# Kernel tuning notes

Measured on AMD Instinct MI355X. Metric: run time of the kernel, lower is better.

## Reference

```python
import jax, jax.numpy as jnp
import numpy as np

EPS = 1e-12
N_POS, N_NEG, N_NEUT, N_ASSAS = 9, 8, 7, 1
VOCAB_K = 512  # vocab_size: number of search results
NEUT_W, NEG_W, ASSAS_W = 1.0, 0.0, -10.0


def _normalize(x):
    # F.normalize(p=2, dim=-1)
    return x / jnp.maximum(jnp.linalg.norm(x, axis=-1, keepdims=True), EPS)


def _pool(embs):
    # mean over dim 1, then L2-normalize
    return _normalize(jnp.mean(embs, axis=1))


def setup_inputs() -> dict:
    key = jax.random.key(0)
    ks = jax.random.split(key, 10)
    B = 64
    inp = {
        "pos_embs": jax.random.normal(ks[0], (B, N_POS, 768), jnp.float32),
        "neg_embs": jax.random.normal(ks[1], (B, N_NEG, 768), jnp.float32),
        "neut_embs": jax.random.normal(ks[2], (B, N_NEUT, 768), jnp.float32),
        "assas_emb": jax.random.normal(ks[3], (B, 768), jnp.float32),
        "vocab_table": jax.random.normal(ks[4], (100000, 768), jnp.float32),
        "W1": jax.random.normal(ks[5], (3072, 2304), jnp.float32) * 0.02,
        "b1": jnp.zeros((2304,), jnp.float32),
        "W2": jax.random.normal(ks[6], (2304, 1700), jnp.float32) * 0.02,
        "b2": jnp.zeros((1700,), jnp.float32),
        "W3": jax.random.normal(ks[7], (1700, 1000), jnp.float32) * 0.02,
        "b3": jnp.zeros((1000,), jnp.float32),
        "W4": jax.random.normal(ks[8], (1000, 768), jnp.float32) * 0.02,
        "b4": jnp.zeros((768,), jnp.float32),
    }
    return inp


def _forward(pos_embs, neg_embs, neut_embs, assas_emb, vocab_table,
             W1, b1, W2, b2, W3, b3, W4, b4):
    # --- combined input: cat(neg_pool, assas, neut_pool, pos_pool) -> [B, 3072]
    concatenated = jnp.concatenate(
        [_pool(neg_embs), assas_emb, _pool(neut_embs), _pool(pos_embs)], axis=1)

    # --- fc MLP with tanh activations (none after last layer)
    h = jnp.tanh(concatenated @ W1 + b1)
    h = jnp.tanh(h @ W2 + b2)
    h = jnp.tanh(h @ W3 + b3)
    model_out = _normalize(h @ W4 + b4)  # [B, 768]

    # --- vocab.search: top-VOCAB_K cosine similarity against vocab table
    vocab_norm = _normalize(vocab_table)            # [N, 768]
    sims = model_out @ vocab_norm.T                  # [B, N]
    _, top_idx = jax.lax.top_k(sims, VOCAB_K)        # [B, V]
    word_embeddings = vocab_table[top_idx]           # [B, V, 768]

    # --- cosine scores against each board group (normalize then dot)
    wn = _normalize(word_embeddings)                 # [B, V, 768]
    pos_s = jnp.einsum('bvd,bpd->bvp', wn, _normalize(pos_embs))    # [B,V,9]
    neg_s = jnp.einsum('bvd,bpd->bvp', wn, _normalize(neg_embs))    # [B,V,8]
    neut_s = jnp.einsum('bvd,bpd->bvp', wn, _normalize(neut_embs))  # [B,V,7]
    assas_s = jnp.einsum('bvd,bd->bv', wn, _normalize(assas_emb))[..., None]  # [B,V,1]

    # --- primary reward: # of positive words ranked before first non-positive
    combined = jnp.concatenate([pos_s, neg_s, neut_s, assas_s], axis=2)  # [B,V,25]
    order = jnp.argsort(-combined, axis=2)           # descending sort indices
    reward_vec = jnp.concatenate(
        [jnp.zeros((N_POS,), jnp.float32),
         jnp.ones((N_NEG + N_NEUT + N_ASSAS,), jnp.float32)])
    rewards = reward_vec[order]                      # [B,V,25]
    primary = jnp.argmax(rewards, axis=2).astype(jnp.float32)  # [B,V]

    # --- secondary reward: weight of the highest-scoring non-positive word
    combined2 = combined[:, :, N_POS:]               # [B,V,16]
    reward_vec2 = jnp.concatenate(
        [jnp.full((N_NEG,), NEG_W, jnp.float32),
         jnp.full((N_NEUT,), NEUT_W, jnp.float32),
         jnp.full((N_ASSAS,), ASSAS_W, jnp.float32)])
    secondary = reward_vec2[jnp.argmax(combined2, axis=2)]      # [B,V]

    tot_reward = primary + secondary                 # [B,V]

    # --- topk(V//2) max / min selection, gather, mean-pool, normalize
    k = VOCAB_K // 2
    _, idx_max = jax.lax.top_k(tot_reward, k)
    _, idx_min = jax.lax.top_k(-tot_reward, k)
    emb_max = jnp.take_along_axis(word_embeddings, idx_max[:, :, None], axis=1)
    emb_min = jnp.take_along_axis(word_embeddings, idx_min[:, :, None], axis=1)
    max_pooled = _pool(emb_max)
    min_pooled = _pool(emb_min)
    search_embedding = emb_max[:, 0]                 # highest-scoring embedding

    return model_out, search_embedding, max_pooled, min_pooled


def reference(pos_embs, neg_embs, neut_embs, assas_emb, vocab_table,
              W1, b1, W2, b2, W3, b3, W4, b4):
    return _forward(pos_embs, neg_embs, neut_embs, assas_emb, vocab_table,
                    W1, b1, W2, b2, W3, b3, W4, b4)
```

## Files before the change

kernel.cpp:

```cpp
#include <hip/hip_runtime.h>
#include <hip/hip_bf16.h>
#include <stdint.h>

#define B_    64
#define D_    768
#define NVOC  100000
#define VK    512
#define KH    256

__device__ __forceinline__ float b2f_raw(unsigned short u) {
    return __uint_as_float(((unsigned int)u) << 16);
}
__device__ __forceinline__ float ldin(const void* p, size_t i, int isbf) {
    return isbf ? b2f_raw(((const unsigned short*)p)[i]) : ((const float*)p)[i];
}
__device__ __forceinline__ float4 ldin4(const void* p, size_t i, int isbf) {
    if (isbf) {
        ushort4 r = *(const ushort4*)((const unsigned short*)p + i);
        return make_float4(b2f_raw(r.x), b2f_raw(r.y), b2f_raw(r.z), b2f_raw(r.w));
    }
    return *(const float4*)((const float*)p + i);
}
__device__ __forceinline__ uint32_t fmono(float x) {
    uint32_t u = __float_as_uint(x);
    return u ^ (uint32_t)((((int32_t)u) >> 31) | 0x80000000u);
}

__device__ __forceinline__ float block_reduce_sum_256(float v, float* red) {
    int tid = threadIdx.x;
    red[tid] = v; __syncthreads();
    #pragma unroll
    for (int s = 128; s > 0; s >>= 1) {
        if (tid < s) red[tid] += red[tid + s];
        __syncthreads();
    }
    float r = red[0]; __syncthreads();
    return r;
}

__global__ void detect_kernel(const void* vocab, int* flag) {
    if (threadIdx.x == 0 && blockIdx.x == 0) {
        const float* vf = (const float*)vocab;
        int sane = 0;
        for (int i = 0; i < 256; i++) {
            float a = fabsf(vf[i]);
            if (a > 1e-4f && a < 64.0f) sane++;
        }
        *flag = (sane >= 200) ? 0 : 1;
    }
}

__global__ __launch_bounds__(256) void prep_kernel(
    const void* __restrict__ pos, const void* __restrict__ neg,
    const void* __restrict__ neut, const void* __restrict__ assas,
    float* __restrict__ concat, float* __restrict__ invemb,
    const int* __restrict__ dflag) {
    __shared__ float red[256];
    int isbf = *dflag;
    int b = blockIdx.x, tid = threadIdx.x;
    int d = tid * 3;
    const void* srcs[3] = {pos, neg, neut};
    const int cnts[3]  = {9, 8, 7};
    const int ieoff[3] = {0, 9, 17};
    const int coff[3]  = {2304, 0, 1536};
    for (int g = 0; g < 3; g++) {
        float m0 = 0.f, m1 = 0.f, m2 = 0.f;
        int cnt = cnts[g];
        for (int m = 0; m < cnt; m++) {
            size_t base = ((size_t)b * cnt + m) * D_ + d;
            float x0 = ldin(srcs[g], base + 0, isbf);
            float x1 = ldin(srcs[g], base + 1, isbf);
            float x2 = ldin(srcs[g], base + 2, isbf);
            float S = block_reduce_sum_256(x0 * x0 + x1 * x1 + x2 * x2, red);
            if (tid == 0)
                invemb[b * 25 + ieoff[g] + m] = 1.0f / fmaxf(sqrtf(S), 1e-12f);
            m0 += x0; m1 += x1; m2 += x2;
        }
        float invc = 1.0f / (float)cnt;
        m0 *= invc; m1 *= invc; m2 *= invc;
        float S = block_reduce_sum_256(m0 * m0 + m1 * m1 + m2 * m2, red);
        float inv = 1.0f / fmaxf(sqrtf(S), 1e-12f);
        float* o = concat + (size_t)b * 3072 + coff[g] + d;
        o[0] = m0 * inv; o[1] = m1 * inv; o[2] = m2 * inv;
    }
    size_t abase = (size_t)b * D_ + d;
    float x0 = ldin(assas, abase + 0, isbf);
    float x1 = ldin(assas, abase + 1, isbf);
    float x2 = ldin(assas, abase + 2, isbf);
    float* oc = concat + (size_t)b * 3072 + 768 + d;
    oc[0] = x0; oc[1] = x1; oc[2] = x2;
    float S = block_reduce_sum_256(x0 * x0 + x1 * x1 + x2 * x2, red);
    if (tid == 0) invemb[b * 25 + 24] = 1.0f / fmaxf(sqrtf(S), 1e-12f);
}

__global__ __launch_bounds__(256) void gemm_partial_kernel(
    const float* __restrict__ X, const void* __restrict__ W,
    float* __restrict__ P, int K, int N, int CH, const int* __restrict__ dflag) {
    __shared__ float xs[64][68];
    __shared__ float wt[64][68];
    int isbf = *dflag;
    int tid = threadIdx.x;
    int n0 = blockIdx.x * 64;
    int kstart = blockIdx.y * CH;
    int kend = min(K, kstart + CH);
    int tx = tid & 15, ty = tid >> 4;
    float acc[4][4] = {{0.f}};
    for (int k0 = kstart; k0 < kend; k0 += 64) {
        #pragma unroll
        for (int q = 0; q < 4; q++) {
            int e4 = tid + q * 256;
            int m = e4 >> 4, kk = (e4 & 15) * 4;
            float4 v = make_float4(0.f, 0.f, 0.f, 0.f);
            if (k0 + kk < kend) v = *(const float4*)(X + (size_t)m * K + k0 + kk);
            xs[kk + 0][m] = v.x; xs[kk + 1][m] = v.y;
            xs[kk + 2][m] = v.z; xs[kk + 3][m] = v.w;
        }
        #pragma unroll
        for (int q = 0; q < 4; q++) {
            int e4 = tid + q * 256;
            int kk = e4 >> 4, c = (e4 & 15) * 4;
            float4 v = make_float4(0.f, 0.f, 0.f, 0.f);
            if (k0 + kk < kend && n0 + c < N)
                v = ldin4(W, (size_t)(k0 + kk) * N + n0 + c, isbf);
            wt[kk][c + 0] = v.x; wt[kk][c + 1] = v.y;
            wt[kk][c + 2] = v.z; wt[kk][c + 3] = v.w;
        }
        __syncthreads();
        #pragma unroll 16
        for (int kk = 0; kk < 64; kk++) {
            float4 a = *(const float4*)&xs[kk][ty * 4];
            float4 w = *(const float4*)&wt[kk][tx * 4];
            acc[0][0] += a.x * w.x; acc[0][1] += a.x * w.y; acc[0][2] += a.x * w.z; acc[0][3] += a.x * w.w;
            acc[1][0] += a.y * w.x; acc[1][1] += a.y * w.y; acc[1][2] += a.y * w.z; acc[1][3] += a.y * w.w;
            acc[2][0] += a.z * w.x; acc[2][1] += a.z * w.y; acc[2][2] += a.z * w.z; acc[2][3] += a.z * w.w;
            acc[3][0] += a.w * w.x; acc[3][1] += a.w * w.y; acc[3][2] += a.w * w.z; acc[3][3] += a.w * w.w;
        }
        __syncthreads();
    }
    size_t base = (size_t)blockIdx.y * 64 * N;
    int n = n0 + tx * 4;
    if (n < N) {
        #pragma unroll
        for (int i = 0; i < 4; i++) {
            float4 o = make_float4(acc[i][0], acc[i][1], acc[i][2], acc[i][3]);
            *(float4*)(P + base + (size_t)(ty * 4 + i) * N + n) = o;
        }
    }
}

__global__ __launch_bounds__(256) void reduce_act_kernel(
    const float* __restrict__ P, const void* __restrict__ bias,
    float* __restrict__ Y, int N, int KS, int act, const int* __restrict__ dflag) {
    int isbf = *dflag;
    int idx = blockIdx.x * 256 + threadIdx.x;
    if (idx >= 64 * N) return;
    int n = idx % N;
    float s = 0.f;
    for (int ks = 0; ks < KS; ks++) s += P[(size_t)ks * 64 * N + idx];
    s += ldin(bias, n, isbf);
    if (act) s = tanhf(s);
    Y[idx] = s;
}

__global__ __launch_bounds__(256) void norm_mo_kernel(
    float* __restrict__ mo, float* __restrict__ out, float* __restrict__ moTp) {
    __shared__ float red[256];
    int b = blockIdx.x, tid = threadIdx.x, d = tid * 3;
    float* r_ = mo + (size_t)b * D_ + d;
    float x0 = r_[0], x1 = r_[1], x2 = r_[2];
    float S = block_reduce_sum_256(x0 * x0 + x1 * x1 + x2 * x2, red);
    float inv = 1.0f / fmaxf(sqrtf(S), 1e-12f);
    x0 *= inv; x1 *= inv; x2 *= inv;
    r_[0] = x0; r_[1] = x1; r_[2] = x2;
    float* o = out + (size_t)b * D_ + d;
    o[0] = x0; o[1] = x1; o[2] = x2;
    if (moTp) {
        moTp[(size_t)(d + 0) * 64 + b] = x0;
        moTp[(size_t)(d + 1) * 64 + b] = x1;
        moTp[(size_t)(d + 2) * 64 + b] = x2;
    }
}

__global__ __launch_bounds__(256) void sims64_kernel(
    const float* __restrict__ moT, const void* __restrict__ vocab,
    float* __restrict__ sims, float* __restrict__ invn,
    const int* __restrict__ dflag) {
    __shared__ float xs[64 * 64];
    __shared__ float wt[64 * 64];
    int isbf = *dflag;
    int tid = threadIdx.x;
    int v0 = blockIdx.x * 64;
    int tx = tid & 15, ty = tid >> 4;
    float acc[4][4] = {{0.f}};
    float ssq[4] = {0.f, 0.f, 0.f, 0.f};
    for (int k0 = 0; k0 < 768; k0 += 64) {
        #pragma unroll
        for (int q = 0; q < 4; q++) {
            int e4 = tid + q * 256;
            int kr = e4 >> 4, m4 = (e4 & 15) * 4;
            float4 v = *(const float4*)(moT + (size_t)(k0 + kr) * 64 + m4);
            *(float4*)&xs[kr * 64 + m4] = v;
        }
        #pragma unroll
        for (int q = 0; q < 4; q++) {
            int e4 = tid + q * 256;
            int r = e4 >> 4, kq = e4 & 15, c = kq * 4;
            float4 v = make_float4(0.f, 0.f, 0.f, 0.f);
            if (v0 + r < NVOC)
                v = ldin4(vocab, (size_t)(v0 + r) * 768 + k0 + c, isbf);
            int colp = r ^ ((kq & 7) << 2);
            wt[(c + 0) * 64 + colp] = v.x;
            wt[(c + 1) * 64 + colp] = v.y;
            wt[(c + 2) * 64 + colp] = v.z;
            wt[(c + 3) * 64 + colp] = v.w;
        }
        __syncthreads();
        #pragma unroll 16
        for (int kk = 0; kk < 64; kk++) {
            float4 a = *(const float4*)&xs[kk * 64 + ty * 4];
            float4 w = *(const float4*)&wt[kk * 64 + ((tx * 4) ^ (((kk >> 2) & 7) << 2))];
            ssq[0] += w.x * w.x; ssq[1] += w.y * w.y; ssq[2] += w.z * w.z; ssq[3] += w.w * w.w;
            acc[0][0] += a.x * w.x; acc[0][1] += a.x * w.y; acc[0][2] += a.x * w.z; acc[0][3] += a.x * w.w;
            acc[1][0] += a.y * w.x; acc[1][1] += a.y * w.y; acc[1][2] += a.y * w.z; acc[1][3] += a.y * w.w;
            acc[2][0] += a.z * w.x; acc[2][1] += a.z * w.y; acc[2][2] += a.z * w.z; acc[2][3] += a.z * w.w;
            acc[3][0] += a.w * w.x; acc[3][1] += a.w * w.y; acc[3][2] += a.w * w.z; acc[3][3] += a.w * w.w;
        }
        __syncthreads();
    }
    int v = v0 + tx * 4;
    if (v < NVOC) {
        float inv[4];
        #pragma unroll
        for (int j = 0; j < 4; j++) inv[j] = 1.0f / fmaxf(sqrtf(ssq[j]), 1e-12f);
        #pragma unroll
        for (int i = 0; i < 4; i++) {
            float4 o = make_float4(acc[i][0] * inv[0], acc[i][1] * inv[1],
                                   acc[i][2] * inv[2], acc[i][3] * inv[3]);
            *(float4*)(sims + (size_t)(ty * 4 + i) * NVOC + v) = o;
        }
        if (ty == 0) *(float4*)(invn + v) = make_float4(inv[0], inv[1], inv[2], inv[3]);
    }
}

__global__ __launch_bounds__(256) void sims_kernel(
    const float* __restrict__ mo32, const void* __restrict__ vocab,
    float* __restrict__ sims, float* __restrict__ invn, int winv,
    const int* __restrict__ dflag) {
    __shared__ float xs[64][36];
    __shared__ float wt[64][68];
    int isbf = *dflag;
    int tid = threadIdx.x;
    int v0 = blockIdx.x * 64;
    int tx = tid & 15, ty = tid >> 4;
    float acc[2][4] = {{0.f}};
    float ssq[4] = {0.f, 0.f, 0.f, 0.f};
    for (int k0 = 0; k0 < 768; k0 += 64) {
        #pragma unroll
        for (int q = 0; q < 2; q++) {
            int e4 = tid + q * 256;
            int m = e4 >> 4, kk = (e4 & 15) * 4;
            float4 v = *(const float4*)(mo32 + (size_t)m * 768 + k0 + kk);
            xs[kk + 0][m] = v.x; xs[kk + 1][m] = v.y;
            xs[kk + 2][m] = v.z; xs[kk + 3][m] = v.w;
        }
        #pragma unroll
        for (int q = 0; q < 4; q++) {
            int e4 = tid + q * 256;
            int r = e4 >> 4, c = (e4 & 15) * 4;
            float4 v = make_float4(0.f, 0.f, 0.f, 0.f);
            if (v0 + r < NVOC)
                v = ldin4(vocab, (size_t)(v0 + r) * 768 + k0 + c, isbf);
            wt[c + 0][r] = v.x; wt[c + 1][r] = v.y;
            wt[c + 2][r] = v.z; wt[c + 3][r] = v.w;
        }
        __syncthreads();
        #pragma unroll 16
        for (int kk = 0; kk < 64; kk++) {
            float2 a = *(const float2*)&xs[kk][ty * 2];
            float4 w = *(const float4*)&wt[kk][tx * 4];
            ssq[0] += w.x * w.x; ssq[1] += w.y * w.y; ssq[2] += w.z * w.z; ssq[3] += w.w * w.w;
            acc[0][0] += a.x * w.x; acc[0][1] += a.x * w.y; acc[0][2] += a.x * w.z; acc[0][3] += a.x * w.w;
            acc[1][0] += a.y * w.x; acc[1][1] += a.y * w.y; acc[1][2] += a.y * w.z; acc[1][3] += a.y * w.w;
        }
        __syncthreads();
    }
    int v = v0 + tx * 4;
    if (v < NVOC) {
        float inv[4];
        #pragma unroll
        for (int j = 0; j < 4; j++) inv[j] = 1.0f / fmaxf(sqrtf(ssq[j]), 1e-12f);
        #pragma unroll
        for (int i = 0; i < 2; i++) {
            float4 o = make_float4(acc[i][0] * inv[0], acc[i][1] * inv[1],
                                   acc[i][2] * inv[2], acc[i][3] * inv[3]);
            *(float4*)(sims + (size_t)(ty * 2 + i) * NVOC + v) = o;
        }
        if (ty == 0 && winv) *(float4*)(invn + v) = make_float4(inv[0], inv[1], inv[2], inv[3]);
    }
}

__device__ void bitonic_desc_u64(unsigned long long* d, int n, int tid, int nt) {
    for (int k = 2; k <= n; k <<= 1) {
        for (int j = k >> 1; j > 0; j >>= 1) {
            for (int i = tid; i < n; i += nt) {
                int ixj = i ^ j;
                if (ixj > i) {
                    unsigned long long a = d[i], b = d[ixj];
                    bool up = ((i & k) == 0);
                    if (up ? (a < b) : (a > b)) { d[i] = b; d[ixj] = a; }
                }
            }
            __syncthreads();
        }
    }
}

__global__ __launch_bounds__(1024) void select512_kernel(
    const float* __restrict__ sims, int* __restrict__ top_idx) {
    __shared__ int hist[4096];
    __shared__ unsigned long long cand[4096];
    __shared__ int ssum[1024];
    __shared__ int s_Tg, s_T, s_cnt;
    int b = blockIdx.x, tid = threadIdx.x;
    const float* row = sims + (size_t)b * NVOC;
    #pragma unroll
    for (int q = 0; q < 4; q++) hist[tid * 4 + q] = 0;
    __syncthreads();
    for (int v = tid; v < NVOC; v += 1024) {
        uint32_t u = fmono(row[v]);
        atomicAdd(&hist[u >> 20], 1);
    }
    __syncthreads();
    int a_ = 0;
    #pragma unroll
    for (int q = 0; q < 4; q++) a_ += hist[tid * 4 + q];
    ssum[tid] = a_; __syncthreads();
    for (int off = 1; off < 1024; off <<= 1) {
        int add = (tid + off < 1024) ? ssum[tid + off] : 0;
        __syncthreads();
        ssum[tid] += add;
        __syncthreads();
    }
    if (ssum[tid] >= VK && (tid == 1023 || ssum[tid + 1] < VK)) s_Tg = tid;
    __syncthreads();
    if (tid == 0) {
        int g = s_Tg;
        int above = (g == 1023) ? 0 : ssum[g + 1];
        int T = g * 4;
        for (int bin = g * 4 + 3; bin >= g * 4; bin--) {
            int c = hist[bin];
            if (above + c >= VK) { T = bin; break; }
            above += c;
        }
        s_T = T; s_cnt = 0;
    }
    __syncthreads();
    uint32_t T = (uint32_t)s_T;
    for (int v = tid; v < NVOC; v += 1024) {
        uint32_t u = fmono(row[v]);
        if ((u >> 20) >= T) {
            int p = atomicAdd(&s_cnt, 1);
            if (p < 4096) cand[p] = ((unsigned long long)u << 32) | (uint32_t)(~v);
        }
    }
    __syncthreads();
    int total = min(s_cnt, 4096);
    for (int i = tid; i < 4096; i += 1024)
        if (i >= total) cand[i] = 0ull;
    __syncthreads();
    bitonic_desc_u64(cand, 4096, tid, 1024);
    if (tid < VK) top_idx[(size_t)b * VK + tid] = (int)(~(uint32_t)(cand[tid] & 0xFFFFFFFFull));
}

__global__ __launch_bounds__(128) void tot_kernel(
    const int* __restrict__ top_idx, const void* __restrict__ vocab,
    const float* __restrict__ invn, const float* __restrict__ invemb,
    const void* __restrict__ pos, const void* __restrict__ neg,
    const void* __restrict__ neut, const void* __restrict__ assas,
    float* __restrict__ tot, const int* __restrict__ dflag) {
    __shared__ float E[25 * 384];
    int isbf = *dflag;
    int b = blockIdx.y;
    int j = blockIdx.x * 128 + threadIdx.x;
    int v = top_idx[(size_t)b * VK + j];
    if ((unsigned)v >= (unsigned)NVOC) v = 0;
    size_t vbase = (size_t)v * D_;
    float p[25];
    #pragma unroll
    for (int i = 0; i < 25; i++) p[i] = 0.f;

    for (int h = 0; h < 2; h++) {
        __syncthreads();
        for (int u = threadIdx.x; u < 2400; u += 128) {
            int i = u / 96;
            int c = (u - i * 96) * 4;
            const void* ep; size_t eb;
            if (i < 9)       { ep = pos;   eb = ((size_t)b * 9 + i) * D_; }
            else if (i < 17) { ep = neg;   eb = ((size_t)b * 8 + (i - 9)) * D_; }
            else if (i < 24) { ep = neut;  eb = ((size_t)b * 7 + (i - 17)) * D_; }
            else             { ep = assas; eb = (size_t)b * D_; }
            float4 x = ldin4(ep, eb + h * 384 + c, isbf);
            float s = invemb[b * 25 + i];
            E[i * 384 + c + 0] = x.x * s;
            E[i * 384 + c + 1] = x.y * s;
            E[i * 384 + c + 2] = x.z * s;
            E[i * 384 + c + 3] = x.w * s;
        }
        __syncthreads();
        for (int c = 0; c < 384; c += 4) {
            float4 w = ldin4(vocab, vbase + h * 384 + c, isbf);
            #pragma unroll
            for (int i = 0; i < 25; i++) {
                float4 e = *(const float4*)&E[i * 384 + c];
                p[i] += w.x * e.x + w.y * e.y + w.z * e.z + w.w * e.w;
            }
        }
    }

    float invv = invn[v];
    #pragma unroll
    for (int i = 0; i < 25; i++) p[i] *= invv;
    float mx = -1e30f; int am = 9;
    #pragma unroll
    for (int i = 9; i < 25; i++) if (p[i] > mx) { mx = p[i]; am = i; }
    int primary = 0;
    #pragma unroll
    for (int i = 0; i < 9; i++) primary += (p[i] >= mx) ? 1 : 0;
    float secondary = (am == 24) ? -10.0f : ((am >= 17) ? 1.0f : 0.0f);
    tot[(size_t)b * VK + j] = (float)primary + secondary;
}

__global__ __launch_bounds__(256) void sort512_kernel(
    const float* __restrict__ tot, int* __restrict__ idx_max, int* __restrict__ idx_min) {
    __shared__ unsigned long long key[512];
    int b = blockIdx.x, tid = threadIdx.x;
    for (int pass = 0; pass < 2; pass++) {
        for (int j = tid; j < 512; j += 256) {
            uint32_t m = fmono(tot[(size_t)b * VK + j]);
            if (pass) m = ~m;
            key[j] = ((unsigned long long)m << 32) | (uint32_t)(511 - j);
        }
        __syncthreads();
        bitonic_desc_u64(key, 512, tid, 256);
        int* dst = pass ? idx_min : idx_max;
        if (tid < 256) dst[(size_t)b * KH + tid] = 511 - (int)(key[tid] & 0xFFFFFFFFull);
        __syncthreads();
    }
}

__global__ __launch_bounds__(256) void pool_kernel(
    const int* __restrict__ top_idx, const int* __restrict__ idx_max,
    const int* __restrict__ idx_min, const void* __restrict__ vocab,
    float* __restrict__ out, const int* __restrict__ dflag) {
    __shared__ float red[256];
    int isbf = *dflag;
    int b = blockIdx.x, s = blockIdx.y, tid = threadIdx.x;
    const int* sel = s ? idx_min : idx_max;
    int d = tid * 3;
    float a0 = 0.f, a1 = 0.f, a2 = 0.f;
    for (int r = 0; r < 256; r++) {
        int v = top_idx[(size_t)b * VK + sel[(size_t)b * KH + r]];
        if ((unsigned)v >= (unsigned)NVOC) v = 0;
        size_t vb = (size_t)v * D_ + d;
        a0 += ldin(vocab, vb + 0, isbf);
        a1 += ldin(vocab, vb + 1, isbf);
        a2 += ldin(vocab, vb + 2, isbf);
    }
    a0 *= (1.0f / 256.0f); a1 *= (1.0f / 256.0f); a2 *= (1.0f / 256.0f);
    float S = block_reduce_sum_256(a0 * a0 + a1 * a1 + a2 * a2, red);
    float inv = 1.0f / fmaxf(sqrtf(S), 1e-12f);
    float* o = out + (size_t)(2 + s) * (B_ * D_) + (size_t)b * D_ + d;
    o[0] = a0 * inv;
    o[1] = a1 * inv;
    o[2] = a2 * inv;
    if (s == 0) {
        int v0 = top_idx[(size_t)b * VK + sel[(size_t)b * KH + 0]];
        if ((unsigned)v0 >= (unsigned)NVOC) v0 = 0;
        size_t vb = (size_t)v0 * D_ + d;
        float* so = out + (size_t)(B_ * D_) + (size_t)b * D_ + d;
        so[0] = ldin(vocab, vb + 0, isbf);
        so[1] = ldin(vocab, vb + 1, isbf);
        so[2] = ldin(vocab, vb + 2, isbf);
    }
}

extern "C" void kernel_launch(void* const* d_in, const int* in_sizes, int n_in,
                              void* d_out, int out_size, void* d_ws, size_t ws_size,
                              hipStream_t stream) {
    const void* pos   = d_in[0];
    const void* neg   = d_in[1];
    const void* neut  = d_in[2];
    const void* assas = d_in[3];
    const void* vocab = d_in[4];
    const void* W1 = d_in[5];  const void* b1 = d_in[6];
    const void* W2 = d_in[7];  const void* b2 = d_in[8];
    const void* W3 = d_in[9];  const void* b3 = d_in[10];
    const void* W4 = d_in[11]; const void* b4 = d_in[12];
    float* out = (float*)d_out;

    int big = ws_size >= (size_t)30 * 1024 * 1024;

    float* ws = (float*)d_ws;
    float* concat = ws;
    float* h1     = concat + 196608;
    float* h2     = h1 + 147456;
    float* h3     = h2 + 108800;
    float* mo     = h3 + 64000;
    float* moT    = mo + 49152;
    float* invn   = big ? (moT + 49152) : moT;
    float* invemb = invn + 100000;
    float* simsPb = invemb + 1600;
    int* top_idx  = (int*)(simsPb + (big ? 6400000 : 3200000));
    float* tot    = (float*)(top_idx + 64 * VK);
    int* imax     = (int*)(tot + 64 * VK);
    int* imin     = imax + 64 * KH;
    int* dflag    = imin + 64 * KH;

    detect_kernel<<<1, 64, 0, stream>>>(vocab, dflag);

    prep_kernel<<<64, 256, 0, stream>>>(pos, neg, neut, assas, concat, invemb, dflag);

    gemm_partial_kernel<<<dim3(36, 8), 256, 0, stream>>>(concat, W1, simsPb, 3072, 2304, 384, dflag);
    reduce_act_kernel<<<576, 256, 0, stream>>>(simsPb, b1, h1, 2304, 8, 1, dflag);
    gemm_partial_kernel<<<dim3(27, 9), 256, 0, stream>>>(h1, W2, simsPb, 2304, 1700, 256, dflag);
    reduce_act_kernel<<<425, 256, 0, stream>>>(simsPb, b2, h2, 1700, 9, 1, dflag);
    gemm_partial_kernel<<<dim3(16, 9), 256, 0, stream>>>(h2, W3, simsPb, 1700, 1000, 192, dflag);
    reduce_act_kernel<<<250, 256, 0, stream>>>(simsPb, b3, h3, 1000, 9, 1, dflag);
    gemm_partial_kernel<<<dim3(12, 8), 256, 0, stream>>>(h3, W4, simsPb, 1000, 768, 128, dflag);
    reduce_act_kernel<<<192, 256, 0, stream>>>(simsPb, b4, mo, 768, 8, 0, dflag);

    norm_mo_kernel<<<64, 256, 0, stream>>>(mo, out, big ? moT : nullptr);

    if (big) {
        sims64_kernel<<<1563, 256, 0, stream>>>(moT, vocab, simsPb, invn, dflag);
        select512_kernel<<<64, 1024, 0, stream>>>(simsPb, top_idx);
    } else {
        for (int pass = 0; pass < 2; pass++) {
            sims_kernel<<<1563, 256, 0, stream>>>(mo + (size_t)pass * 32 * D_, vocab,
                                                  simsPb, invn, pass == 0, dflag);
            select512_kernel<<<32, 1024, 0, stream>>>(simsPb, top_idx + (size_t)pass * 32 * VK);
        }
    }

    tot_kernel<<<dim3(4, 64), 128, 0, stream>>>(top_idx, vocab, invn, invemb,
                                                pos, neg, neut, assas, tot, dflag);

    sort512_kernel<<<64, 256, 0, stream>>>(tot, imax, imin);

    pool_kernel<<<dim3(64, 2), 256, 0, stream>>>(top_idx, imax, imin, vocab, out, dflag);
}
```

Measured before the change: 1.084 ms.

## Add bf16 MFMA similarity path and split top-512 selection into partitions

Adds a bf16 MFMA similarity kernel that splits the normalized model output into hi/lo bf16 halves, so vocab tables stored as bf16 can use matrix cores. It only runs when the input-dtype flag says bf16. The fp32 tiled kernel is kept and now runs only for fp32 inputs. Separately, the single-block-per-row top-512 selection is replaced by a 4-way partitioned histogram select plus a bitonic merge kernel. This raises the number of blocks working on selection, at the cost of an extra launch, more workspace, and a raised workspace threshold for the big path.

```diff
diff --git a/kernel.cpp b/kernel.cpp
--- a/kernel.cpp
+++ b/kernel.cpp
@@ -7,6 +7,11 @@
 #define NVOC  100000
 #define VK    512
 #define KH    256
+#define NPART 4
+#define PLEN  25000
+
+typedef __attribute__((ext_vector_type(8))) short short8v;
+typedef __attribute__((ext_vector_type(4))) float f32x4;
 
 __device__ __forceinline__ float b2f_raw(unsigned short u) {
     return __uint_as_float(((unsigned int)u) << 16);
@@ -20,6 +25,11 @@
         return make_float4(b2f_raw(r.x), b2f_raw(r.y), b2f_raw(r.z), b2f_raw(r.w));
     }
     return *(const float4*)((const float*)p + i);
+}
+__device__ __forceinline__ unsigned short f2bf(float x) {
+    uint32_t u = __float_as_uint(x);
+    uint32_t r = (u + 0x7FFFu + ((u >> 16) & 1u)) >> 16;
+    return (unsigned short)r;
 }
 __device__ __forceinline__ uint32_t fmono(float x) {
     uint32_t u = __float_as_uint(x);
@@ -163,7 +173,8 @@
 }
 
 __global__ __launch_bounds__(256) void norm_mo_kernel(
-    float* __restrict__ mo, float* __restrict__ out, float* __restrict__ moTp) {
+    float* __restrict__ mo, float* __restrict__ out, float* __restrict__ moTp,
+    unsigned short* __restrict__ moA) {
     __shared__ float red[256];
     int b = blockIdx.x, tid = threadIdx.x, d = tid * 3;
     float* r_ = mo + (size_t)b * D_ + d;
@@ -179,15 +190,109 @@
         moTp[(size_t)(d + 1) * 64 + b] = x1;
         moTp[(size_t)(d + 2) * 64 + b] = x2;
     }
+    if (moA) {
+        float xv[3] = {x0, x1, x2};
+        int w = b >> 4;
+        #pragma unroll
+        for (int c = 0; c < 3; c++) {
+            int k = d + c;
+            float x = xv[c];
+            unsigned short hi = f2bf(x);
+            unsigned short lo = f2bf(x - b2f_raw(hi));
+            int kb2 = k >> 5, sub = (k >> 3) & 3, e = k & 7;
+            int lane = (b & 15) | (sub << 4);
+            moA[((((0 * 24 + kb2) * 4 + w) * 64) + lane) * 8 + e] = hi;
+            moA[((((1 * 24 + kb2) * 4 + w) * 64) + lane) * 8 + e] = lo;
+        }
+    }
+}
+
+__global__ __launch_bounds__(256) void sims64_mfma_kernel(
+    const unsigned short* __restrict__ moA, const void* __restrict__ vocab,
+    float* __restrict__ sims, float* __restrict__ invn,
+    const int* __restrict__ dflag) {
+    if (*dflag != 1) return;
+    __shared__ unsigned short Bt[4096];
+    __shared__ float invLds[64];
+    const unsigned short* voc = (const unsigned short*)vocab;
+    int tid = threadIdx.x;
+    int v0 = blockIdx.x * 64;
+    int w = tid >> 6, lane = tid & 63;
+    f32x4 acc[4];
+    #pragma unroll
+    for (int i = 0; i < 4; i++) acc[i] = (f32x4){0.f, 0.f, 0.f, 0.f};
+    float ssqA = 0.f, ssqB = 0.f;
+    int srow = tid >> 3;
+    int scc  = tid & 7;
+    for (int kb = 0; kb < 12; kb++) {
+        #pragma unroll
+        for (int q = 0; q < 2; q++) {
+            int row = srow + q * 32;
+            uint4 r = make_uint4(0u, 0u, 0u, 0u);
+            if (v0 + row < NVOC)
+                r = *(const uint4*)(voc + (size_t)(v0 + row) * 768 + kb * 64 + scc * 8);
+            float s = 0.f;
+            uint32_t us[4] = {r.x, r.y, r.z, r.w};
+            #pragma unroll
+            for (int t2 = 0; t2 < 4; t2++) {
+                float f0 = __uint_as_float(us[t2] << 16);
+                float f1 = __uint_as_float(us[t2] & 0xFFFF0000u);
+                s += f0 * f0 + f1 * f1;
+            }
+            if (q == 0) ssqA += s; else ssqB += s;
+            *(uint4*)&Bt[(scc * 64 + row) * 8] = r;
+        }
+        __syncthreads();
+        #pragma unroll
+        for (int ks = 0; ks < 2; ks++) {
+            int kb2 = kb * 2 + ks;
+            short8v ah = *(const short8v*)&moA[((((0 * 24 + kb2) * 4 + w) * 64) + lane) * 8];
+            short8v al = *(const short8v*)&moA[((((1 * 24 + kb2) * 4 + w) * 64) + lane) * 8];
+            int cc = ks * 4 + (lane >> 4);
+            #pragma unroll
+            for (int vs = 0; vs < 4; vs++) {
+                int row = vs * 16 + (lane & 15);
+                short8v bf = *(const short8v*)&Bt[(cc * 64 + row) * 8];
+                acc[vs] = __builtin_amdgcn_mfma_f32_16x16x32_bf16(ah, bf, acc[vs], 0, 0, 0);
+                acc[vs] = __builtin_amdgcn_mfma_f32_16x16x32_bf16(al, bf, acc[vs], 0, 0, 0);
+            }
+        }
+        __syncthreads();
+    }
+    #pragma unroll
+    for (int off = 1; off < 8; off <<= 1) {
+        ssqA += __shfl_xor(ssqA, off, 64);
+        ssqB += __shfl_xor(ssqB, off, 64);
+    }
+    if (scc == 0) {
+        float iA = 1.0f / fmaxf(sqrtf(ssqA), 1e-12f);
+        float iB = 1.0f / fmaxf(sqrtf(ssqB), 1e-12f);
+        invLds[srow] = iA; invLds[srow + 32] = iB;
+        if (v0 + srow < NVOC)      invn[v0 + srow] = iA;
+        if (v0 + srow + 32 < NVOC) invn[v0 + srow + 32] = iB;
+    }
+    __syncthreads();
+    #pragma unroll
+    for (int vs = 0; vs < 4; vs++) {
+        int v = v0 + vs * 16 + (lane & 15);
+        if (v < NVOC) {
+            float iv = invLds[vs * 16 + (lane & 15)];
+            #pragma unroll
+            for (int reg = 0; reg < 4; reg++) {
+                int m = w * 16 + (lane >> 4) * 4 + reg;
+                sims[(size_t)m * NVOC + v] = acc[vs][reg] * iv;
+            }
+        }
+    }
 }
 
 __global__ __launch_bounds__(256) void sims64_kernel(
     const float* __restrict__ moT, const void* __restrict__ vocab,
     float* __restrict__ sims, float* __restrict__ invn,
     const int* __restrict__ dflag) {
+    if (*dflag != 0) return;
     __shared__ float xs[64 * 64];
     __shared__ float wt[64 * 64];
-    int isbf = *dflag;
     int tid = threadIdx.x;
     int v0 = blockIdx.x * 64;
     int tx = tid & 15, ty = tid >> 4;
@@ -207,7 +312,7 @@
             int r = e4 >> 4, kq = e4 & 15, c = kq * 4;
             float4 v = make_float4(0.f, 0.f, 0.f, 0.f);
             if (v0 + r < NVOC)
-                v = ldin4(vocab, (size_t)(v0 + r) * 768 + k0 + c, isbf);
+                v = *(const float4*)((const float*)vocab + (size_t)(v0 + r) * 768 + k0 + c);
             int colp = r ^ ((kq & 7) << 2);
             wt[(c + 0) * 64 + colp] = v.x;
             wt[(c + 1) * 64 + colp] = v.y;
@@ -313,6 +418,76 @@
             __syncthreads();
         }
     }
+}
+
+__global__ __launch_bounds__(1024) void pselect_kernel(
+    const float* __restrict__ sims, unsigned long long* __restrict__ psel) {
+    __shared__ int hist[4096];
+    __shared__ unsigned long long cand[2048];
+    __shared__ int ssum[1024];
+    __shared__ int s_Tg, s_T, s_cnt;
+    int b = blockIdx.y, part = blockIdx.x, tid = threadIdx.x;
+    const float* row = sims + (size_t)b * NVOC + (size_t)part * PLEN;
+    #pragma unroll
+    for (int q = 0; q < 4; q++) hist[tid * 4 + q] = 0;
+    __syncthreads();
+    for (int v = tid; v < PLEN; v += 1024) {
+        uint32_t u = fmono(row[v]);
+        atomicAdd(&hist[u >> 20], 1);
+    }
+    __syncthreads();
+    int a_ = 0;
+    #pragma unroll
+    for (int q = 0; q < 4; q++) a_ += hist[tid * 4 + q];
+    ssum[tid] = a_; __syncthreads();
+    for (int off = 1; off < 1024; off <<= 1) {
+        int add = (tid + off < 1024) ? ssum[tid + off] : 0;
+        __syncthreads();
+        ssum[tid] += add;
+        __syncthreads();
+    }
+    if (ssum[tid] >= VK && (tid == 1023 || ssum[tid + 1] < VK)) s_Tg = tid;
+    __syncthreads();
+    if (tid == 0) {
+        int g = s_Tg;
+        int above = (g == 1023) ? 0 : ssum[g + 1];
+        int T = g * 4;
+        for (int bin = g * 4 + 3; bin >= g * 4; bin--) {
+            int c = hist[bin];
+            if (above + c >= VK) { T = bin; break; }
+            above += c;
+        }
+        s_T = T; s_cnt = 0;
+    }
+    __syncthreads();
+    uint32_t T = (uint32_t)s_T;
+    for (int v = tid; v < PLEN; v += 1024) {
+        uint32_t u = fmono(row[v]);
+        if ((u >> 20) >= T) {
+            int p = atomicAdd(&s_cnt, 1);
+            if (p < 2048) {
+                uint32_t vg = (uint32_t)(part * PLEN + v);
+                cand[p] = ((unsigned long long)u << 32) | (uint32_t)(~vg);
+            }
+        }
+    }
+    __syncthreads();
+    int total = min(s_cnt, 2048);
+    for (int i = tid; i < 2048; i += 1024)
+        if (i >= total) cand[i] = 0ull;
+    __syncthreads();
+    bitonic_desc_u64(cand, 2048, tid, 1024);
+    if (tid < VK) psel[((size_t)b * NPART + part) * VK + tid] = cand[tid];
+}
+
+__global__ __launch_bounds__(512) void pmerge_kernel(
+    const unsigned long long* __restrict__ psel, int* __restrict__ top_idx) {
+    __shared__ unsigned long long key[2048];
+    int b = blockIdx.x, tid = threadIdx.x;
+    for (int i = tid; i < 2048; i += 512) key[i] = psel[(size_t)b * 2048 + i];
+    __syncthreads();
+    bitonic_desc_u64(key, 2048, tid, 512);
+    if (tid < VK) top_idx[(size_t)b * VK + tid] = (int)(~(uint32_t)(key[tid] & 0xFFFFFFFFull));
 }
 
 __global__ __launch_bounds__(1024) void select512_kernel(
@@ -498,54 +673,90 @@
     const void* W4 = d_in[11]; const void* b4 = d_in[12];
     float* out = (float*)d_out;
 
-    int big = ws_size >= (size_t)30 * 1024 * 1024;
+    int big = ws_size >= (size_t)32 * 1024 * 1024;
 
     float* ws = (float*)d_ws;
-    float* concat = ws;
-    float* h1     = concat + 196608;
-    float* h2     = h1 + 147456;
-    float* h3     = h2 + 108800;
-    float* mo     = h3 + 64000;
-    float* moT    = mo + 49152;
-    float* invn   = big ? (moT + 49152) : moT;
-    float* invemb = invn + 100000;
-    float* simsPb = invemb + 1600;
-    int* top_idx  = (int*)(simsPb + (big ? 6400000 : 3200000));
-    float* tot    = (float*)(top_idx + 64 * VK);
-    int* imax     = (int*)(tot + 64 * VK);
-    int* imin     = imax + 64 * KH;
-    int* dflag    = imin + 64 * KH;
-
-    detect_kernel<<<1, 64, 0, stream>>>(vocab, dflag);
-
-    prep_kernel<<<64, 256, 0, stream>>>(pos, neg, neut, assas, concat, invemb, dflag);
-
-    gemm_partial_kernel<<<dim3(36, 8), 256, 0, stream>>>(concat, W1, simsPb, 3072, 2304, 384, dflag);
-    reduce_act_kernel<<<576, 256, 0, stream>>>(simsPb, b1, h1, 2304, 8, 1, dflag);
-    gemm_partial_kernel<<<dim3(27, 9), 256, 0, stream>>>(h1, W2, simsPb, 2304, 1700, 256, dflag);
-    reduce_act_kernel<<<425, 256, 0, stream>>>(simsPb, b2, h2, 1700, 9, 1, dflag);
-    gemm_partial_kernel<<<dim3(16, 9), 256, 0, stream>>>(h2, W3, simsPb, 1700, 1000, 192, dflag);
-    reduce_act_kernel<<<250, 256, 0, stream>>>(simsPb, b3, h3, 1000, 9, 1, dflag);
-    gemm_partial_kernel<<<dim3(12, 8), 256, 0, stream>>>(h3, W4, simsPb, 1000, 768, 128, dflag);
-    reduce_act_kernel<<<192, 256, 0, stream>>>(simsPb, b4, mo, 768, 8, 0, dflag);
-
-    norm_mo_kernel<<<64, 256, 0, stream>>>(mo, out, big ? moT : nullptr);
-
     if (big) {
+        float* concat = ws;
+        float* h1     = concat + 196608;
+        float* h2     = h1 + 147456;
+        float* h3     = h2 + 108800;
+        float* mo     = h3 + 64000;
+        float* moT    = mo + 49152;
+        float* moA_f  = moT + 49152;
+        float* invn   = moA_f + 49152;
+        float* invemb = invn + 100000;
+        float* simsPb = invemb + 1600;
+        int* top_idx  = (int*)(simsPb + 6400000);
+        float* tot    = (float*)(top_idx + 64 * VK);
+        int* imax     = (int*)(tot + 64 * VK);
+        int* imin     = imax + 64 * KH;
+        unsigned long long* psel = (unsigned long long*)(imin + 64 * KH);
+        int* dflag    = (int*)(psel + 64 * NPART * VK);
+        unsigned short* moAu = (unsigned short*)moA_f;
+
+        detect_kernel<<<1, 64, 0, stream>>>(vocab, dflag);
+        prep_kernel<<<64, 256, 0, stream>>>(pos, neg, neut, assas, concat, invemb, dflag);
+
+        gemm_partial_kernel<<<dim3(36, 8), 256, 0, stream>>>(concat, W1, simsPb, 3072, 2304, 384, dflag);
+        reduce_act_kernel<<<576, 256, 0, stream>>>(simsPb, b1, h1, 2304, 8, 1, dflag);
+        gemm_partial_kernel<<<dim3(27, 9), 256, 0, stream>>>(h1, W2, simsPb, 2304, 1700, 256, dflag);
+        reduce_act_kernel<<<425, 256, 0, stream>>>(simsPb, b2, h2, 1700, 9, 1, dflag);
+        gemm_partial_kernel<<<dim3(16, 9), 256, 0, stream>>>(h2, W3, simsPb, 1700, 1000, 192, dflag);
+        reduce_act_kernel<<<250, 256, 0, stream>>>(simsPb, b3, h3, 1000, 9, 1, dflag);
+        gemm_partial_kernel<<<dim3(12, 8), 256, 0, stream>>>(h3, W4, simsPb, 1000, 768, 128, dflag);
+        reduce_act_kernel<<<192, 256, 0, stream>>>(simsPb, b4, mo, 768, 8, 0, dflag);
+
+        norm_mo_kernel<<<64, 256, 0, stream>>>(mo, out, moT, moAu);
+
+        sims64_mfma_kernel<<<1563, 256, 0, stream>>>(moAu, vocab, simsPb, invn, dflag);
         sims64_kernel<<<1563, 256, 0, stream>>>(moT, vocab, simsPb, invn, dflag);
-        select512_kernel<<<64, 1024, 0, stream>>>(simsPb, top_idx);
+
+        pselect_kernel<<<dim3(NPART, 64), 1024, 0, stream>>>(simsPb, psel);
+        pmerge_kernel<<<64, 512, 0, stream>>>(psel, top_idx);
+
+        tot_kernel<<<dim3(4, 64), 128, 0, stream>>>(top_idx, vocab, invn, invemb,
+                                                    pos, neg, neut, assas, tot, dflag);
+        sort512_kernel<<<64, 256, 0, stream>>>(tot, imax, imin);
+        pool_kernel<<<dim3(64, 2), 256, 0, stream>>>(top_idx, imax, imin, vocab, out, dflag);
     } else {
+        float* concat = ws;
+        float* h1     = concat + 196608;
+        float* h2     = h1 + 147456;
+        float* h3     = h2 + 108800;
+        float* mo     = h3 + 64000;
+        float* invn   = mo + 49152;
+        float* invemb = invn + 100000;
+        float* simsPb = invemb + 1600;
+        int* top_idx  = (int*)(simsPb + 3200000);
+        float* tot    = (float*)(top_idx + 64 * VK);
+        int* imax     = (int*)(tot + 64 * VK);
+        int* imin     = imax + 64 * KH;
+        int* dflag    = imin + 64 * KH;
+
+        detect_kernel<<<1, 64, 0, stream>>>(vocab, dflag);
+        prep_kernel<<<64, 256, 0, stream>>>(pos, neg, neut, assas, concat, invemb, dflag);
+
+        gemm_partial_kernel<<<dim3(36, 8), 256, 0, stream>>>(concat, W1, simsPb, 3072, 2304, 384, dflag);
+        reduce_act_kernel<<<576, 256, 0, stream>>>(simsPb, b1, h1, 2304, 8, 1, dflag);
+        gemm_partial_kernel<<<dim3(27, 9), 256, 0, stream>>>(h1, W2, simsPb, 2304, 1700, 256, dflag);
+        reduce_act_kernel<<<425, 256, 0, stream>>>(simsPb, b2, h2, 1700, 9, 1, dflag);
+        gemm_partial_kernel<<<dim3(16, 9), 256, 0, stream>>>(h2, W3, simsPb, 1700, 1000, 192, dflag);
+        reduce_act_kernel<<<250, 256, 0, stream>>>(simsPb, b3, h3, 1000, 9, 1, dflag);
+        gemm_partial_kernel<<<dim3(12, 8), 256, 0, stream>>>(h3, W4, simsPb, 1000, 768, 128, dflag);
+        reduce_act_kernel<<<192, 256, 0, stream>>>(simsPb, b4, mo, 768, 8, 0, dflag);
+
+        norm_mo_kernel<<<64, 256, 0, stream>>>(mo, out, nullptr, nullptr);
+
         for (int pass = 0; pass < 2; pass++) {
             sims_kernel<<<1563, 256, 0, stream>>>(mo + (size_t)pass * 32 * D_, vocab,
                                                   simsPb, invn, pass == 0, dflag);
             select512_kernel<<<32, 1024, 0, stream>>>(simsPb, top_idx + (size_t)pass * 32 * VK);
         }
-    }
-
-    tot_kernel<<<dim3(4, 64), 128, 0, stream>>>(top_idx, vocab, invn, invemb,
-                                                pos, neg, neut, assas, tot, dflag);
-
-    sort512_kernel<<<64, 256, 0, stream>>>(tot, imax, imin);
-
-    pool_kernel<<<dim3(64, 2), 256, 0, stream>>>(top_idx, imax, imin, vocab, out, dflag);
-}
+
+        tot_kernel<<<dim3(4, 64), 128, 0, stream>>>(top_idx, vocab, invn, invemb,
+                                                    pos, neg, neut, assas, tot, dflag);
+        sort512_kernel<<<64, 256, 0, stream>>>(tot, imax, imin);
+        pool_kernel<<<dim3(64, 2), 256, 0, stream>>>(top_idx, imax, imin, vocab, out, dflag);
+    }
+}
```

New measurement: 1.063 ms. About the same (-1.9%).
